# Optimization experiments

Measured on AMD Instinct MI355X. Metric: run time of the kernel, lower is better.

The kernel has to match this reference:

```python
import jax, jax.numpy as jnp
import numpy as np

L, E, NH, V, BS = 8, 1024, 16, 32000, 1024  # layers, embed, heads, vocab, block_size
HD = E // NH  # head dim = 64
FF = 4 * E


def layernorm(x, scale, bias, eps=1e-5):
    mu = jnp.mean(x, axis=-1, keepdims=True)
    var = jnp.var(x, axis=-1, keepdims=True)
    return (x - mu) * jax.lax.rsqrt(var + eps) * scale + bias


def setup_inputs() -> dict:
    key = jax.random.key(0)
    ks = jax.random.split(key, 16)
    s = 0.02
    B, T = 2, 1024
    return {
        "idx": jax.random.randint(ks[0], (B, T), 0, V),
        "tok_emb": jax.random.normal(ks[1], (V, E), jnp.float32) * s,
        "pos_emb": jax.random.normal(ks[2], (BS, E), jnp.float32) * s,
        "Wq": jax.random.normal(ks[3], (L, E, E), jnp.float32) * s,
        "Wk": jax.random.normal(ks[4], (L, E, E), jnp.float32) * s,
        "Wv": jax.random.normal(ks[5], (L, E, E), jnp.float32) * s,
        "Wo": jax.random.normal(ks[6], (L, E, E), jnp.float32) * s,
        "bo": jnp.zeros((L, E), jnp.float32),
        "ln1_s": jnp.ones((L, E), jnp.float32),
        "ln1_b": jnp.zeros((L, E), jnp.float32),
        "W1": jax.random.normal(ks[7], (L, E, FF), jnp.float32) * s,
        "b1": jnp.zeros((L, FF), jnp.float32),
        "W2": jax.random.normal(ks[8], (L, FF, E), jnp.float32) * s,
        "b2": jnp.zeros((L, E), jnp.float32),
        "ln2_s": jnp.ones((L, E), jnp.float32),
        "ln2_b": jnp.zeros((L, E), jnp.float32),
        "lnf_s": jnp.ones((E,), jnp.float32),
        "lnf_b": jnp.zeros((E,), jnp.float32),
        "lm_w": jax.random.normal(ks[9], (E, V), jnp.float32) * s,
        "lm_b": jnp.zeros((V,), jnp.float32),
    }


def reference(idx, tok_emb, pos_emb, Wq, Wk, Wv, Wo, bo, ln1_s, ln1_b,
              W1, b1, W2, b2, ln2_s, ln2_b, lnf_s, lnf_b, lm_w, lm_b):
    B, T = idx.shape
    x = tok_emb[idx] + pos_emb[:T]  # [B,T,E]
    causal = jnp.triu(jnp.ones((T, T), bool), 1)  # True above diagonal -> masked
    scale = 1.0 / jnp.sqrt(jnp.asarray(HD, x.dtype))
    for l in range(L):
        h = layernorm(x, ln1_s[l], ln1_b[l])
        q = (h @ Wq[l]).reshape(B, T, NH, HD)
        k = (h @ Wk[l]).reshape(B, T, NH, HD)
        v = (h @ Wv[l]).reshape(B, T, NH, HD)
        scores = jnp.einsum("bthd,bshd->bhts", q, k) * scale  # [B,H,T,T]
        scores = jnp.where(causal, -jnp.inf, scores)
        attn = jax.nn.softmax(scores, axis=-1)
        o = jnp.einsum("bhts,bshd->bthd", attn, v).reshape(B, T, E)
        x = x + o @ Wo[l] + bo[l]
        h2 = layernorm(x, ln2_s[l], ln2_b[l])
        x = x + jax.nn.gelu(h2 @ W1[l] + b1[l], approximate=False) @ W2[l] + b2[l]
    x = layernorm(x, lnf_s, lnf_b)
    logits = x @ lm_w + lm_b  # [B,T,V]
    return logits
```

## Files before the change

kernel.cpp:

```cpp
#include <hip/hip_runtime.h>

#define EDIM 1024
#define NHEADS 16
#define HDIM 64
#define TSEQ 1024
#define NBATCH 2
#define MROWS 2048
#define FFDIM 4096
#define NLAYERS 8
#define VOCAB 32000
#define QKVN 3072
#define SC2 0.18033688011112042f

typedef __attribute__((ext_vector_type(4))) float f32x4;
typedef __attribute__((ext_vector_type(8))) short short8;

__device__ __forceinline__ unsigned short f2bf(float f) {
    union { float f; unsigned u; } v; v.f = f;
    unsigned r = v.u + 0x7fffu + ((v.u >> 16) & 1u);
    return (unsigned short)(r >> 16);
}

__device__ __forceinline__ f32x4 mfma_bf16(short8 a, short8 b, f32x4 c) {
    return __builtin_amdgcn_mfma_f32_16x16x32_bf16(a, b, c, 0, 0, 0);
}

__device__ __forceinline__ void gload16(const unsigned short* g, unsigned short* l) {
    __builtin_amdgcn_global_load_lds(
        (const __attribute__((address_space(1))) unsigned int*)g,
        (__attribute__((address_space(3))) unsigned int*)l, 16, 0, 0);
}

__device__ __forceinline__ void ln_store(
    f32x4 v, int tid, const float* __restrict__ sc, const float* __restrict__ bi,
    unsigned short* __restrict__ hrow)
{
    float sum = v[0] + v[1] + v[2] + v[3];
    float sq = v[0]*v[0] + v[1]*v[1] + v[2]*v[2] + v[3]*v[3];
    #pragma unroll
    for (int m = 1; m <= 32; m <<= 1) { sum += __shfl_xor(sum, m); sq += __shfl_xor(sq, m); }
    __shared__ float sh[8];
    int w = tid >> 6;
    if ((tid & 63) == 0) { sh[w] = sum; sh[4 + w] = sq; }
    __syncthreads();
    sum = sh[0] + sh[1] + sh[2] + sh[3];
    sq  = sh[4] + sh[5] + sh[6] + sh[7];
    float mu = sum * (1.0f / EDIM);
    float inv = rsqrtf(sq * (1.0f / EDIM) - mu * mu + 1e-5f);
    int c = tid * 4;
    unsigned o0 = (unsigned)f2bf((v[0] - mu) * inv * sc[c + 0] + bi[c + 0])
                | ((unsigned)f2bf((v[1] - mu) * inv * sc[c + 1] + bi[c + 1]) << 16);
    unsigned o1 = (unsigned)f2bf((v[2] - mu) * inv * sc[c + 2] + bi[c + 2])
                | ((unsigned)f2bf((v[3] - mu) * inv * sc[c + 3] + bi[c + 3]) << 16);
    unsigned* hp = (unsigned*)(hrow + c);
    hp[0] = o0; hp[1] = o1;
}

__global__ __launch_bounds__(256) void embed_ln_kernel(
    const int* __restrict__ idx, const float* __restrict__ tok,
    const float* __restrict__ pos, float* __restrict__ x,
    const float* __restrict__ sc, const float* __restrict__ bi,
    unsigned short* __restrict__ h)
{
    int row = blockIdx.x, tid = threadIdx.x;
    int t = row & (TSEQ - 1);
    int tokid = idx[row];
    int c = tid * 4;
    f32x4 a = *(const f32x4*)(tok + (size_t)tokid * EDIM + c);
    f32x4 b = *(const f32x4*)(pos + (size_t)t * EDIM + c);
    f32x4 v = a + b;
    *(f32x4*)(x + (size_t)row * EDIM + c) = v;
    ln_store(v, tid, sc, bi, h + (size_t)row * EDIM);
}

template<int KZ>
__global__ __launch_bounds__(256) void reduce_ln_kernel(
    const float* __restrict__ part, const float* __restrict__ bias,
    float* __restrict__ x, const float* __restrict__ sc,
    const float* __restrict__ bi, unsigned short* __restrict__ h)
{
    int row = blockIdx.x, tid = threadIdx.x;
    int c = tid * 4;
    f32x4 s = *(const f32x4*)(x + (size_t)row * EDIM + c);
    s += *(const f32x4*)(bias + c);
    #pragma unroll
    for (int kz = 0; kz < KZ; ++kz)
        s += *(const f32x4*)(part + ((size_t)kz * MROWS + row) * EDIM + c);
    *(f32x4*)(x + (size_t)row * EDIM + c) = s;
    ln_store(s, tid, sc, bi, h + (size_t)row * EDIM);
}

__device__ __forceinline__ void conv_tile(
    unsigned short* __restrict__ Tb,
    const float* __restrict__ W, unsigned short* __restrict__ WT,
    int Kdim, int Ndim, int k0, int n0, int tid)
{
    int r = tid >> 4, c4 = (tid & 15) * 4;
    #pragma unroll
    for (int i = 0; i < 4; ++i) {
        f32x4 v = *(const f32x4*)(W + (size_t)(k0 + r + 16 * i) * Ndim + n0 + c4);
        Tb[(c4 + 0) * 72 + r + 16 * i] = f2bf(v[0]);
        Tb[(c4 + 1) * 72 + r + 16 * i] = f2bf(v[1]);
        Tb[(c4 + 2) * 72 + r + 16 * i] = f2bf(v[2]);
        Tb[(c4 + 3) * 72 + r + 16 * i] = f2bf(v[3]);
    }
    __syncthreads();
    int nr = tid >> 2, kc = (tid & 3) * 16;
    short8 o0 = *(const short8*)&Tb[nr * 72 + kc];
    short8 o1 = *(const short8*)&Tb[nr * 72 + kc + 8];
    *(short8*)(WT + (size_t)(n0 + nr) * Kdim + k0 + kc)     = o0;
    *(short8*)(WT + (size_t)(n0 + nr) * Kdim + k0 + kc + 8) = o1;
}

__device__ __forceinline__ void wconv_layer_body(
    unsigned short* Tb, int t, int tid,
    const float* Wq, const float* Wk, const float* Wv, const float* Wo,
    const float* W1, const float* W2,
    unsigned short* qkvT, unsigned short* woT,
    unsigned short* w1T, unsigned short* w2T)
{
    if (t < 768) {
        int wsel = t >> 8, tt = t & 255;
        const float* src = wsel == 0 ? Wq : (wsel == 1 ? Wk : Wv);
        conv_tile(Tb, src, qkvT + (size_t)wsel * EDIM * EDIM, EDIM, EDIM,
                  (tt & 15) * 64, (tt >> 4) * 64, tid);
    } else if (t < 1024) {
        int tt = t - 768;
        conv_tile(Tb, Wo, woT, EDIM, EDIM, (tt & 15) * 64, (tt >> 4) * 64, tid);
    } else if (t < 2048) {
        int tt = t - 1024;
        conv_tile(Tb, W1, w1T, EDIM, FFDIM, (tt & 15) * 64, (tt >> 4) * 64, tid);
    } else {
        int tt = t - 2048;
        conv_tile(Tb, W2, w2T, FFDIM, EDIM, (tt >> 4) * 64, (tt & 15) * 64, tid);
    }
}

__global__ __launch_bounds__(256) void wconv_layer_kernel(
    const float* __restrict__ Wq, const float* __restrict__ Wk,
    const float* __restrict__ Wv, const float* __restrict__ Wo,
    const float* __restrict__ W1, const float* __restrict__ W2,
    unsigned short* __restrict__ qkvT, unsigned short* __restrict__ woT,
    unsigned short* __restrict__ w1T, unsigned short* __restrict__ w2T)
{
    __shared__ __align__(16) unsigned short Tb[64 * 72];
    wconv_layer_body(Tb, blockIdx.x, threadIdx.x, Wq, Wk, Wv, Wo, W1, W2,
                     qkvT, woT, w1T, w2T);
}

__global__ __launch_bounds__(256) void wconv_kernel(
    const float* __restrict__ W, unsigned short* __restrict__ WT, int Kdim, int Ndim)
{
    __shared__ __align__(16) unsigned short Tb[64 * 72];
    conv_tile(Tb, W, WT, Kdim, Ndim, blockIdx.x * 64, blockIdx.y * 64, threadIdx.x);
}

template<int EPI>
__device__ __forceinline__ void gemm128_body(
    unsigned short* SMEM,
    const unsigned short* __restrict__ A, const unsigned short* __restrict__ WT,
    float* __restrict__ Cf, unsigned short* __restrict__ Cb,
    int Ndim, int Kdim, int ntiles, int nwg, int kspan, int bid, int kz)
{
    unsigned short* A_lds = SMEM;
    unsigned short* B_lds = SMEM + 8192;
    int tid = threadIdx.x;
    int q8 = nwg >> 3;
    int swz = (bid & 7) * q8 + (bid >> 3);
    int bm0 = (swz / ntiles) * 128, bn0 = (swz % ntiles) * 128;
    int lane = tid & 63, w = tid >> 6;
    int wr = w >> 1, wc = w & 1;
    int r16 = lane & 15, cc = lane >> 4;
    int lrow = lane >> 3;
    int lcol = ((lane & 7) ^ lrow) * 8;
    int sw = r16 & 7;

    f32x4 acc[4][4];
    #pragma unroll
    for (int m = 0; m < 4; ++m)
        #pragma unroll
        for (int n = 0; n < 4; ++n) acc[m][n] = {0.f, 0.f, 0.f, 0.f};

    int kbeg = kz * kspan, kend = kbeg + kspan;
    for (int k0 = kbeg; k0 < kend; k0 += 64) {
        #pragma unroll
        for (int i = 0; i < 4; ++i) {
            int c = i * 4 + w;
            gload16(A + (size_t)(bm0 + c * 8 + lrow) * Kdim + k0 + lcol, A_lds + c * 512);
            gload16(WT + (size_t)(bn0 + c * 8 + lrow) * Kdim + k0 + lcol, B_lds + c * 512);
        }
        __syncthreads();
        #pragma unroll
        for (int kh = 0; kh < 2; ++kh) {
            short8 af[4], bfr[4];
            #pragma unroll
            for (int m = 0; m < 4; ++m)
                af[m] = *(const short8*)&A_lds[(wr * 64 + m * 16 + r16) * 64 + ((kh * 4 + cc) ^ sw) * 8];
            #pragma unroll
            for (int n = 0; n < 4; ++n)
                bfr[n] = *(const short8*)&B_lds[(wc * 64 + n * 16 + r16) * 64 + ((kh * 4 + cc) ^ sw) * 8];
            #pragma unroll
            for (int m = 0; m < 4; ++m)
                #pragma unroll
                for (int n = 0; n < 4; ++n)
                    acc[m][n] = mfma_bf16(af[m], bfr[n], acc[m][n]);
        }
        __syncthreads();
    }

    #pragma unroll
    for (int m = 0; m < 4; ++m) {
        #pragma unroll
        for (int n = 0; n < 4; ++n) {
            #pragma unroll
            for (int j = 0; j < 4; ++j) {
                int row = bm0 + wr * 64 + m * 16 + cc * 4 + j;
                int col = bn0 + wc * 64 + n * 16 + r16;
                float vv = acc[m][n][j];
                if constexpr (EPI == 0)
                    Cb[(size_t)row * Ndim + col] = f2bf(vv);
                else
                    (Cf + (size_t)kz * MROWS * Ndim)[(size_t)row * Ndim + col] = vv;
            }
        }
    }
}

template<int EPI>
__global__ __launch_bounds__(256, 3) void gemm128(
    const unsigned short* __restrict__ A, const unsigned short* __restrict__ WT,
    float* __restrict__ Cf, unsigned short* __restrict__ Cb,
    int Ndim, int Kdim, int ntiles, int nwg, int kspan)
{
    __shared__ __align__(16) unsigned short SMEM[16384];
    gemm128_body<EPI>(SMEM, A, WT, Cf, Cb, Ndim, Kdim, ntiles, nwg, kspan,
                      blockIdx.x, blockIdx.y);
}

template<int MODE>
__global__ __launch_bounds__(256, 3) void ff2_fused_kernel(
    const unsigned short* __restrict__ A, const unsigned short* __restrict__ WT,
    float* __restrict__ Cf,
    const float* __restrict__ Wq, const float* __restrict__ Wk,
    const float* __restrict__ Wv, const float* __restrict__ Wo,
    const float* __restrict__ W1, const float* __restrict__ W2,
    const float* __restrict__ lmW,
    unsigned short* __restrict__ qkvT, unsigned short* __restrict__ woT,
    unsigned short* __restrict__ w1T, unsigned short* __restrict__ w2Tn,
    unsigned short* __restrict__ lmT)
{
    __shared__ __align__(16) unsigned short SMEM[16384];
    int bid = blockIdx.x;
    if (bid < 512) {
        gemm128_body<4>(SMEM, A, WT, Cf, nullptr, EDIM, FFDIM, 8, 128, 1024,
                        bid & 127, bid >> 7);
    } else if constexpr (MODE == 0) {
        wconv_layer_body(SMEM, bid - 512, threadIdx.x, Wq, Wk, Wv, Wo, W1, W2,
                         qkvT, woT, w1T, w2Tn);
    } else {
        int t = bid - 512;
        conv_tile(SMEM, lmW, lmT, EDIM, VOCAB, (t & 15) * 64, (t >> 4) * 64, threadIdx.x);
    }
}

template<int EPI>
__global__ __launch_bounds__(512, 2) void gemm_p3(
    const unsigned short* __restrict__ A, const unsigned short* __restrict__ WT,
    const float* __restrict__ bias, float* __restrict__ Cf,
    unsigned short* __restrict__ Cb, int Ndim, int Kdim, int mtiles, int ntiles)
{
    __shared__ __align__(16) unsigned short LDS[3][24576];
    const int tid = threadIdx.x;
    const int nwg = mtiles * ntiles, q8 = nwg >> 3;
    const int swz = (int)(blockIdx.x & 7) * q8 + (int)(blockIdx.x >> 3);
    const int bn0 = (swz / mtiles) * 256, bm0 = (swz % mtiles) * 128;
    const int lane = tid & 63, w = tid >> 6;
    const int wr = w >> 2, wc = w & 3;
    const int r16 = lane & 15, cc = lane >> 4;
    const int lrow = lane >> 3;
    const int lcol = ((lane & 7) ^ lrow) * 8;
    const int sw = r16 & 7;

    f32x4 acc[4][4];
    #pragma unroll
    for (int m = 0; m < 4; ++m)
        #pragma unroll
        for (int n = 0; n < 4; ++n) acc[m][n] = {0.f, 0.f, 0.f, 0.f};

    const int nk = Kdim >> 6;

    auto STAGE = [&](int t, int bufidx) {
        int k0 = t * 64;
        unsigned short* buf = &LDS[bufidx][0];
        #pragma unroll
        for (int i = 0; i < 2; ++i) {
            int c = i * 8 + w;
            gload16(A + (size_t)(bm0 + c * 8 + lrow) * Kdim + k0 + lcol, buf + c * 512);
        }
        #pragma unroll
        for (int i = 0; i < 4; ++i) {
            int c = i * 8 + w;
            gload16(WT + (size_t)(bn0 + c * 8 + lrow) * Kdim + k0 + lcol, buf + 8192 + c * 512);
        }
    };

    STAGE(0, 0);
    STAGE(1, 1);
    asm volatile("s_waitcnt vmcnt(6)" ::: "memory");
    __builtin_amdgcn_sched_barrier(0);
    __builtin_amdgcn_s_barrier();
    __builtin_amdgcn_sched_barrier(0);

    int cur = 0;
    for (int t = 0; t < nk; ++t) {
        if (t + 2 < nk) STAGE(t + 2, cur == 0 ? 2 : cur - 1);
        const unsigned short* Abuf = &LDS[cur][0];
        const unsigned short* Bbuf = &LDS[cur][8192];
        #pragma unroll
        for (int kh = 0; kh < 2; ++kh) {
            short8 af[4], bfr[4];
            #pragma unroll
            for (int m = 0; m < 4; ++m)
                af[m] = *(const short8*)&Abuf[(wr * 64 + m * 16 + r16) * 64 + ((kh * 4 + cc) ^ sw) * 8];
            #pragma unroll
            for (int n = 0; n < 4; ++n)
                bfr[n] = *(const short8*)&Bbuf[(wc * 64 + n * 16 + r16) * 64 + ((kh * 4 + cc) ^ sw) * 8];
            __builtin_amdgcn_s_setprio(1);
            #pragma unroll
            for (int m = 0; m < 4; ++m)
                #pragma unroll
                for (int n = 0; n < 4; ++n)
                    acc[m][n] = mfma_bf16(af[m], bfr[n], acc[m][n]);
            __builtin_amdgcn_s_setprio(0);
        }
        if (t + 1 < nk) {
            if (t + 2 < nk) asm volatile("s_waitcnt vmcnt(6)" ::: "memory");
            else            asm volatile("s_waitcnt vmcnt(0)" ::: "memory");
            __builtin_amdgcn_sched_barrier(0);
            __builtin_amdgcn_s_barrier();
            __builtin_amdgcn_sched_barrier(0);
            asm volatile("" ::: "memory");
        }
        cur = cur == 2 ? 0 : cur + 1;
    }

    #pragma unroll
    for (int m = 0; m < 4; ++m) {
        #pragma unroll
        for (int n = 0; n < 4; ++n) {
            #pragma unroll
            for (int j = 0; j < 4; ++j) {
                int row = bm0 + wr * 64 + m * 16 + cc * 4 + j;
                int col = bn0 + wc * 64 + n * 16 + r16;
                float vv = acc[m][n][j] + bias[col];
                if constexpr (EPI == 2) {
                    vv = 0.5f * vv * (1.0f + erff(vv * 0.70710678118654752f));
                    Cb[(size_t)row * Ndim + col] = f2bf(vv);
                } else {
                    Cf[(size_t)row * Ndim + col] = vv;
                }
            }
        }
    }
}

__global__ __launch_bounds__(256, 2) void gemm_wide_lm(
    const unsigned short* __restrict__ A, const unsigned short* __restrict__ WT,
    const float* __restrict__ bias, float* __restrict__ Cf,
    int Ndim, int Kdim, int mtiles, int ntiles)
{
    __shared__ __align__(16) unsigned short A_lds[128][64];
    __shared__ __align__(16) unsigned short B_lds[256][64];
    int tid = threadIdx.x;
    int nwg = mtiles * ntiles;
    int q8 = nwg >> 3;
    int swz = (int)(blockIdx.x & 7) * q8 + (int)(blockIdx.x >> 3);
    int bn0 = (swz / mtiles) * 256, bm0 = (swz % mtiles) * 128;
    int lane = tid & 63, w = tid >> 6;
    int wr = w >> 1, wc = w & 1;
    int r16 = lane & 15, cc = lane >> 4;
    int lrow = lane >> 3;
    int lcol = ((lane & 7) ^ lrow) * 8;
    int sw = r16 & 7;

    f32x4 acc[4][8];
    #pragma unroll
    for (int m = 0; m < 4; ++m)
        #pragma unroll
        for (int n = 0; n < 8; ++n) acc[m][n] = {0.f, 0.f, 0.f, 0.f};

    for (int k0 = 0; k0 < Kdim; k0 += 64) {
        #pragma unroll
        for (int i = 0; i < 4; ++i) {
            int c = i * 4 + w;
            gload16(A + (size_t)(bm0 + c * 8 + lrow) * Kdim + k0 + lcol,
                    (unsigned short*)A_lds + c * 512);
        }
        #pragma unroll
        for (int i = 0; i < 8; ++i) {
            int c = i * 4 + w;
            gload16(WT + (size_t)(bn0 + c * 8 + lrow) * Kdim + k0 + lcol,
                    (unsigned short*)B_lds + c * 512);
        }
        __syncthreads();
        #pragma unroll
        for (int kh = 0; kh < 2; ++kh) {
            short8 af[4], bfr[8];
            #pragma unroll
            for (int m = 0; m < 4; ++m)
                af[m] = *(const short8*)&A_lds[wr * 64 + m * 16 + r16][((kh * 4 + cc) ^ sw) * 8];
            #pragma unroll
            for (int n = 0; n < 8; ++n)
                bfr[n] = *(const short8*)&B_lds[wc * 128 + n * 16 + r16][((kh * 4 + cc) ^ sw) * 8];
            #pragma unroll
            for (int m = 0; m < 4; ++m)
                #pragma unroll
                for (int n = 0; n < 8; ++n)
                    acc[m][n] = mfma_bf16(af[m], bfr[n], acc[m][n]);
        }
        __syncthreads();
    }

    #pragma unroll
    for (int m = 0; m < 4; ++m) {
        #pragma unroll
        for (int n = 0; n < 8; ++n) {
            #pragma unroll
            for (int j = 0; j < 4; ++j) {
                int row = bm0 + wr * 64 + m * 16 + cc * 4 + j;
                int col = bn0 + wc * 128 + n * 16 + r16;
                Cf[(size_t)row * Ndim + col] = acc[m][n][j] + bias[col];
            }
        }
    }
}

__global__ __launch_bounds__(256) void attn_kernel(
    const unsigned short* __restrict__ qkv, unsigned short* __restrict__ o)
{
    __shared__ __align__(16) unsigned short K_lds[128][72];
    __shared__ __align__(16) unsigned short VT_lds[64][136];
    __shared__ __align__(16) unsigned short P_lds[4][16][136];

    int qt = (int)gridDim.x - 1 - (int)blockIdx.x;
    int head = blockIdx.y, bb = blockIdx.z;
    int tid = threadIdx.x, w = tid >> 6, lane = tid & 63;
    int r16 = lane & 15, cc = lane >> 4;
    size_t base = ((size_t)bb * TSEQ) * QKVN + head * HDIM;
    const unsigned short* q = qkv + base;
    const unsigned short* k = qkv + base + EDIM;
    const unsigned short* v = qkv + base + 2 * EDIM;
    size_t obase = ((size_t)bb * TSEQ) * EDIM + head * HDIM;
    int qbase = qt * 64;

    const unsigned short* qp = q + (size_t)(qbase + w * 16 + r16) * QKVN;
    short8 aq0 = *(const short8*)(qp + cc * 8);
    short8 aq1 = *(const short8*)(qp + 32 + cc * 8);

    f32x4 oacc[4];
    float m2[4], lrow[4];
    #pragma unroll
    for (int n = 0; n < 4; ++n) oacc[n] = {0.f, 0.f, 0.f, 0.f};
    #pragma unroll
    for (int j = 0; j < 4; ++j) { m2[j] = -1e30f; lrow[j] = 0.f; }

    int krow = tid >> 1, kch = (tid & 1) * 32;
    int vk2 = (tid & 63) * 2, vdb = (tid >> 6) * 16;

    int nkt = (qt + 2) >> 1;
    for (int kt = 0; kt < nkt; ++kt) {
        int kbase = kt * 128;
        const unsigned short* kp = k + (size_t)(kbase + krow) * QKVN + kch;
        *(short8*)&K_lds[krow][kch]      = *(const short8*)kp;
        *(short8*)&K_lds[krow][kch + 8]  = *(const short8*)(kp + 8);
        *(short8*)&K_lds[krow][kch + 16] = *(const short8*)(kp + 16);
        *(short8*)&K_lds[krow][kch + 24] = *(const short8*)(kp + 24);
        const unsigned short* vp0 = v + (size_t)(kbase + vk2) * QKVN + vdb;
        short8 v0a = *(const short8*)vp0;
        short8 v0b = *(const short8*)(vp0 + 8);
        short8 v1a = *(const short8*)(vp0 + QKVN);
        short8 v1b = *(const short8*)(vp0 + QKVN + 8);
        #pragma unroll
        for (int i = 0; i < 8; ++i) {
            *(unsigned*)&VT_lds[vdb + i][vk2] =
                (unsigned)(unsigned short)v0a[i] | ((unsigned)(unsigned short)v1a[i] << 16);
            *(unsigned*)&VT_lds[vdb + 8 + i][vk2] =
                (unsigned)(unsigned short)v0b[i] | ((unsigned)(unsigned short)v1b[i] << 16);
        }
        __syncthreads();

        f32x4 s[8];
        __builtin_amdgcn_s_setprio(1);
        #pragma unroll
        for (int n = 0; n < 8; ++n) {
            short8 bk0 = *(const short8*)&K_lds[n * 16 + r16][cc * 8];
            short8 bk1 = *(const short8*)&K_lds[n * 16 + r16][32 + cc * 8];
            f32x4 z = {0.f, 0.f, 0.f, 0.f};
            z = mfma_bf16(aq0, bk0, z);
            z = mfma_bf16(aq1, bk1, z);
            s[n] = z;
        }
        __builtin_amdgcn_s_setprio(0);
        int myrow = qbase + w * 16 + cc * 4;
        #pragma unroll
        for (int n = 0; n < 8; ++n) {
            int key = kbase + n * 16 + r16;
            #pragma unroll
            for (int j = 0; j < 4; ++j) {
                float sv = s[n][j] * SC2;
                if (key > myrow + j) sv = -1e30f;
                s[n][j] = sv;
            }
        }
        float tmax[4];
        #pragma unroll
        for (int j = 0; j < 4; ++j) {
            float t0 = fmaxf(fmaxf(s[0][j], s[1][j]), fmaxf(s[2][j], s[3][j]));
            float t1 = fmaxf(fmaxf(s[4][j], s[5][j]), fmaxf(s[6][j], s[7][j]));
            float tm = fmaxf(t0, t1);
            #pragma unroll
            for (int mm = 1; mm <= 8; mm <<= 1) tm = fmaxf(tm, __shfl_xor(tm, mm));
            tmax[j] = tm;
        }
        bool defer = (tmax[0] - m2[0] <= 11.5f) && (tmax[1] - m2[1] <= 11.5f)
                  && (tmax[2] - m2[2] <= 11.5f) && (tmax[3] - m2[3] <= 11.5f);
        if (!__all(defer)) {
            #pragma unroll
            for (int j = 0; j < 4; ++j) {
                float mnew = fmaxf(m2[j], tmax[j]);
                float al = exp2f(m2[j] - mnew);
                m2[j] = mnew;
                lrow[j] *= al;
                #pragma unroll
                for (int n = 0; n < 4; ++n) oacc[n][j] *= al;
            }
        }
        #pragma unroll
        for (int j = 0; j < 4; ++j) {
            float ts = 0.f;
            #pragma unroll
            for (int n = 0; n < 8; ++n) {
                float pe = exp2f(s[n][j] - m2[j]);
                s[n][j] = pe;
                ts += pe;
            }
            #pragma unroll
            for (int mm = 1; mm <= 8; mm <<= 1) ts += __shfl_xor(ts, mm);
            lrow[j] += ts;
        }
        #pragma unroll
        for (int n = 0; n < 8; ++n)
            #pragma unroll
            for (int j = 0; j < 4; ++j)
                P_lds[w][cc * 4 + j][n * 16 + r16] = f2bf(s[n][j]);
        short8 pa[4];
        #pragma unroll
        for (int qq = 0; qq < 4; ++qq)
            pa[qq] = *(const short8*)&P_lds[w][r16][qq * 32 + cc * 8];
        __builtin_amdgcn_s_setprio(1);
        #pragma unroll
        for (int n = 0; n < 4; ++n) {
            #pragma unroll
            for (int qq = 0; qq < 4; ++qq) {
                short8 bv = *(const short8*)&VT_lds[n * 16 + r16][qq * 32 + cc * 8];
                oacc[n] = mfma_bf16(pa[qq], bv, oacc[n]);
            }
        }
        __builtin_amdgcn_s_setprio(0);
        __syncthreads();
    }
    float rl[4];
    #pragma unroll
    for (int j = 0; j < 4; ++j) rl[j] = 1.0f / lrow[j];
    #pragma unroll
    for (int n = 0; n < 4; ++n)
        #pragma unroll
        for (int j = 0; j < 4; ++j) {
            int row = qbase + w * 16 + cc * 4 + j;
            o[obase + (size_t)row * EDIM + n * 16 + r16] = f2bf(oacc[n][j] * rl[j]);
        }
}

extern "C" void kernel_launch(void* const* d_in, const int* in_sizes, int n_in,
                              void* d_out, int out_size, void* d_ws, size_t ws_size,
                              hipStream_t stream) {
    const int*   idx     = (const int*)d_in[0];
    const float* tok_emb = (const float*)d_in[1];
    const float* pos_emb = (const float*)d_in[2];
    const float* Wq      = (const float*)d_in[3];
    const float* Wk      = (const float*)d_in[4];
    const float* Wv      = (const float*)d_in[5];
    const float* Wo      = (const float*)d_in[6];
    const float* bo      = (const float*)d_in[7];
    const float* ln1_s   = (const float*)d_in[8];
    const float* ln1_b   = (const float*)d_in[9];
    const float* W1      = (const float*)d_in[10];
    const float* b1      = (const float*)d_in[11];
    const float* W2      = (const float*)d_in[12];
    const float* b2      = (const float*)d_in[13];
    const float* ln2_s   = (const float*)d_in[14];
    const float* ln2_b   = (const float*)d_in[15];
    const float* lnf_s   = (const float*)d_in[16];
    const float* lnf_b   = (const float*)d_in[17];
    const float* lm_w    = (const float*)d_in[18];
    const float* lm_b    = (const float*)d_in[19];
    float* out = (float*)d_out;

    const size_t MB = 1 << 20;
    char* ws = (char*)d_ws;
    float*          x    = (float*)ws;
    unsigned short* h    = (unsigned short*)(ws + 8 * MB);
    unsigned short* qkv  = (unsigned short*)(ws + 12 * MB);
    unsigned short* ao   = (unsigned short*)(ws + 24 * MB);
    unsigned short* ff   = (unsigned short*)(ws + 28 * MB);
    unsigned short* qkvT = (unsigned short*)(ws + 44 * MB);
    unsigned short* woT  = (unsigned short*)(ws + 50 * MB);
    unsigned short* w1T  = (unsigned short*)(ws + 52 * MB);
    unsigned short* w2Ta = (unsigned short*)(ws + 60 * MB);
    unsigned short* lmT  = (unsigned short*)(ws + 68 * MB);

    bool tier1 = ws_size >= (size_t)140 * MB;
    bool tier2 = ws_size >= (size_t)172 * MB;
    unsigned short* w2Tb = tier1 ? (unsigned short*)(ws + 131 * MB) : w2Ta;
    float* part = (float*)(ws + (tier2 ? (size_t)139 * MB : (size_t)68 * MB));

    dim3 blk(256);
    embed_ln_kernel<<<MROWS, blk, 0, stream>>>(idx, tok_emb, pos_emb, x, ln1_s, ln1_b, h);
    wconv_layer_kernel<<<3072, blk, 0, stream>>>(Wq, Wk, Wv, Wo, W1, W2,
                                                 qkvT, woT, w1T, w2Ta);

    for (int l = 0; l < NLAYERS; ++l) {
        unsigned short* w2cur = (l & 1) ? w2Tb : w2Ta;
        unsigned short* w2nxt = ((l + 1) & 1) ? w2Tb : w2Ta;
        size_t eo1 = (size_t)(l + 1) * EDIM * EDIM;

        gemm128<0><<<dim3(384, 1), blk, 0, stream>>>(h, qkvT, nullptr, qkv, QKVN, EDIM, 24, 384, EDIM);
        attn_kernel<<<dim3(TSEQ / 64, NHEADS, NBATCH), blk, 0, stream>>>(qkv, ao);
        gemm128<4><<<dim3(128, 4), blk, 0, stream>>>(ao, woT, part, nullptr, EDIM, EDIM, 8, 128, 256);
        reduce_ln_kernel<4><<<MROWS, blk, 0, stream>>>(part, bo + l * EDIM, x, ln2_s + l * EDIM, ln2_b + l * EDIM, h);
        gemm_p3<2><<<dim3(256, 1), dim3(512), 0, stream>>>(h, w1T, b1 + l * FFDIM, nullptr, ff, FFDIM, EDIM, 16, 16);
        if (l < NLAYERS - 1) {
            if (tier1)
                ff2_fused_kernel<0><<<3584, blk, 0, stream>>>(
                    ff, w2cur, part,
                    Wq + eo1, Wk + eo1, Wv + eo1, Wo + eo1,
                    W1 + (size_t)(l + 1) * EDIM * FFDIM, W2 + (size_t)(l + 1) * FFDIM * EDIM,
                    nullptr, qkvT, woT, w1T, w2nxt, nullptr);
            else {
                gemm128<4><<<dim3(128, 4), blk, 0, stream>>>(ff, w2cur, part, nullptr, EDIM, FFDIM, 8, 128, 1024);
                wconv_layer_kernel<<<3072, blk, 0, stream>>>(
                    Wq + eo1, Wk + eo1, Wv + eo1, Wo + eo1,
                    W1 + (size_t)(l + 1) * EDIM * FFDIM, W2 + (size_t)(l + 1) * FFDIM * EDIM,
                    qkvT, woT, w1T, w2nxt);
            }
        } else {
            if (tier2)
                ff2_fused_kernel<1><<<8512, blk, 0, stream>>>(
                    ff, w2cur, part,
                    nullptr, nullptr, nullptr, nullptr, nullptr, nullptr,
                    lm_w, nullptr, nullptr, nullptr, nullptr, lmT);
            else
                gemm128<4><<<dim3(128, 4), blk, 0, stream>>>(ff, w2cur, part, nullptr, EDIM, FFDIM, 8, 128, 1024);
        }
        if (l < NLAYERS - 1)
            reduce_ln_kernel<4><<<MROWS, blk, 0, stream>>>(part, b2 + l * EDIM, x, ln1_s + (l + 1) * EDIM, ln1_b + (l + 1) * EDIM, h);
        else
            reduce_ln_kernel<4><<<MROWS, blk, 0, stream>>>(part, b2 + l * EDIM, x, lnf_s, lnf_b, h);
    }
    if (!tier2)
        wconv_kernel<<<dim3(16, 500), blk, 0, stream>>>(lm_w, lmT, EDIM, VOCAB);
    gemm_wide_lm<<<dim3(2000, 1), blk, 0, stream>>>(h, lmT, lm_b, out, VOCAB, EDIM, 16, 125);
}
```

Measured before the change: 1.455 ms.

## Rewrite LM-head GEMM as 256x256 tile, 8-wave, triple-buffered pipelined kernel

Replaces the 128x256 LM-head GEMM with a 512-thread kernel that computes 256x256 tiles. It streams K in 32-wide slices through a three-stage LDS ring buffer and issues global loads for step t+2 while MFMAs run on step t. It also raises wave priority around the MFMA bursts and uses explicit vmcnt waits with barriers. The goals are more operand reuse per tile and hiding global-load latency behind compute. In exchange it runs one block per CU with a large register footprint, launches fewer workgroups (1000), and depends on the hand-tuned wait counts being correct.

```diff
diff --git a/kernel.cpp b/kernel.cpp
--- a/kernel.cpp
+++ b/kernel.cpp
@@ -364,71 +364,109 @@
     }
 }
 
-__global__ __launch_bounds__(256, 2) void gemm_wide_lm(
+__global__ __launch_bounds__(512, 1) void gemm_8p(
     const unsigned short* __restrict__ A, const unsigned short* __restrict__ WT,
     const float* __restrict__ bias, float* __restrict__ Cf,
     int Ndim, int Kdim, int mtiles, int ntiles)
 {
-    __shared__ __align__(16) unsigned short A_lds[128][64];
-    __shared__ __align__(16) unsigned short B_lds[256][64];
-    int tid = threadIdx.x;
-    int nwg = mtiles * ntiles;
-    int q8 = nwg >> 3;
-    int swz = (int)(blockIdx.x & 7) * q8 + (int)(blockIdx.x >> 3);
-    int bn0 = (swz / mtiles) * 256, bm0 = (swz % mtiles) * 128;
-    int lane = tid & 63, w = tid >> 6;
-    int wr = w >> 1, wc = w & 1;
-    int r16 = lane & 15, cc = lane >> 4;
-    int lrow = lane >> 3;
-    int lcol = ((lane & 7) ^ lrow) * 8;
-    int sw = r16 & 7;
-
-    f32x4 acc[4][8];
-    #pragma unroll
-    for (int m = 0; m < 4; ++m)
-        #pragma unroll
-        for (int n = 0; n < 8; ++n) acc[m][n] = {0.f, 0.f, 0.f, 0.f};
-
-    for (int k0 = 0; k0 < Kdim; k0 += 64) {
-        #pragma unroll
-        for (int i = 0; i < 4; ++i) {
-            int c = i * 4 + w;
-            gload16(A + (size_t)(bm0 + c * 8 + lrow) * Kdim + k0 + lcol,
-                    (unsigned short*)A_lds + c * 512);
-        }
-        #pragma unroll
-        for (int i = 0; i < 8; ++i) {
-            int c = i * 4 + w;
-            gload16(WT + (size_t)(bn0 + c * 8 + lrow) * Kdim + k0 + lcol,
-                    (unsigned short*)B_lds + c * 512);
-        }
-        __syncthreads();
-        #pragma unroll
-        for (int kh = 0; kh < 2; ++kh) {
-            short8 af[4], bfr[8];
-            #pragma unroll
-            for (int m = 0; m < 4; ++m)
-                af[m] = *(const short8*)&A_lds[wr * 64 + m * 16 + r16][((kh * 4 + cc) ^ sw) * 8];
-            #pragma unroll
-            for (int n = 0; n < 8; ++n)
-                bfr[n] = *(const short8*)&B_lds[wc * 128 + n * 16 + r16][((kh * 4 + cc) ^ sw) * 8];
-            #pragma unroll
-            for (int m = 0; m < 4; ++m)
-                #pragma unroll
-                for (int n = 0; n < 8; ++n)
-                    acc[m][n] = mfma_bf16(af[m], bfr[n], acc[m][n]);
-        }
-        __syncthreads();
-    }
-
-    #pragma unroll
-    for (int m = 0; m < 4; ++m) {
-        #pragma unroll
-        for (int n = 0; n < 8; ++n) {
+    __shared__ __align__(16) unsigned short LDS[3][16384];
+    const int tid = threadIdx.x;
+    const int nwg = mtiles * ntiles, q8 = nwg >> 3;
+    const int swz = (int)(blockIdx.x & 7) * q8 + (int)(blockIdx.x >> 3);
+    const int bn0 = (swz / mtiles) * 256, bm0 = (swz % mtiles) * 256;
+    const int lane = tid & 63, w = tid >> 6;
+    const int wr = w >> 2, wc = w & 3;
+    const int r16 = lane & 15, cc = lane >> 4;
+
+    f32x4 acc[8][4];
+    #pragma unroll
+    for (int m = 0; m < 8; ++m)
+        #pragma unroll
+        for (int n = 0; n < 4; ++n) acc[m][n] = {0.f, 0.f, 0.f, 0.f};
+
+    const int nk = Kdim >> 5;
+
+    #pragma unroll
+    for (int tt = 0; tt < 2; ++tt) {
+        int k0 = tt * 32;
+        unsigned short* buf = &LDS[tt][0];
+        #pragma unroll
+        for (int i = 0; i < 2; ++i) {
+            int c = w * 2 + i;
+            gload16(A  + (size_t)(bm0 + c * 16 + r16) * Kdim + k0 + cc * 8, buf + c * 512);
+            gload16(WT + (size_t)(bn0 + c * 16 + r16) * Kdim + k0 + cc * 8, buf + 8192 + c * 512);
+        }
+    }
+    asm volatile("s_waitcnt vmcnt(4)" ::: "memory");
+    __builtin_amdgcn_sched_barrier(0);
+    __builtin_amdgcn_s_barrier();
+    __builtin_amdgcn_sched_barrier(0);
+
+    int cur = 0;
+    for (int t = 0; t < nk; ++t) {
+        const unsigned short* Abuf = &LDS[cur][0];
+        const unsigned short* Bbuf = &LDS[cur][8192];
+        int nxt = cur + 2; if (nxt >= 3) nxt -= 3;
+        int k2 = (t + 2) * 32;
+        short8 bf[4], af0[4];
+        #pragma unroll
+        for (int n = 0; n < 4; ++n)
+            bf[n] = *(const short8*)(Bbuf + (wc * 4 + n) * 512 + lane * 8);
+        #pragma unroll
+        for (int m = 0; m < 4; ++m)
+            af0[m] = *(const short8*)(Abuf + (wr * 8 + m) * 512 + lane * 8);
+        if (t + 2 < nk) {
+            unsigned short* buf = &LDS[nxt][0];
+            #pragma unroll
+            for (int i = 0; i < 2; ++i) {
+                int c = w * 2 + i;
+                gload16(A + (size_t)(bm0 + c * 16 + r16) * Kdim + k2 + cc * 8, buf + c * 512);
+            }
+        }
+        __builtin_amdgcn_s_setprio(1);
+        #pragma unroll
+        for (int m = 0; m < 4; ++m)
+            #pragma unroll
+            for (int n = 0; n < 4; ++n)
+                acc[m][n] = mfma_bf16(af0[m], bf[n], acc[m][n]);
+        __builtin_amdgcn_s_setprio(0);
+        short8 af1[4];
+        #pragma unroll
+        for (int m = 0; m < 4; ++m)
+            af1[m] = *(const short8*)(Abuf + (wr * 8 + 4 + m) * 512 + lane * 8);
+        if (t + 2 < nk) {
+            unsigned short* buf = &LDS[nxt][8192];
+            #pragma unroll
+            for (int i = 0; i < 2; ++i) {
+                int c = w * 2 + i;
+                gload16(WT + (size_t)(bn0 + c * 16 + r16) * Kdim + k2 + cc * 8, buf + c * 512);
+            }
+        }
+        __builtin_amdgcn_s_setprio(1);
+        #pragma unroll
+        for (int m = 0; m < 4; ++m)
+            #pragma unroll
+            for (int n = 0; n < 4; ++n)
+                acc[4 + m][n] = mfma_bf16(af1[m], bf[n], acc[4 + m][n]);
+        __builtin_amdgcn_s_setprio(0);
+        if (t + 1 < nk) {
+            if (t + 2 < nk) asm volatile("s_waitcnt vmcnt(4)" ::: "memory");
+            else            asm volatile("s_waitcnt vmcnt(0)" ::: "memory");
+            __builtin_amdgcn_sched_barrier(0);
+            __builtin_amdgcn_s_barrier();
+            __builtin_amdgcn_sched_barrier(0);
+        }
+        cur = cur + 1; if (cur >= 3) cur -= 3;
+    }
+
+    #pragma unroll
+    for (int m = 0; m < 8; ++m) {
+        #pragma unroll
+        for (int n = 0; n < 4; ++n) {
             #pragma unroll
             for (int j = 0; j < 4; ++j) {
-                int row = bm0 + wr * 64 + m * 16 + cc * 4 + j;
-                int col = bn0 + wc * 128 + n * 16 + r16;
+                int row = bm0 + wr * 128 + m * 16 + cc * 4 + j;
+                int col = bn0 + wc * 64 + n * 16 + r16;
                 Cf[(size_t)row * Ndim + col] = acc[m][n][j] + bias[col];
             }
         }
@@ -669,5 +707,5 @@
     }
     if (!tier2)
         wconv_kernel<<<dim3(16, 500), blk, 0, stream>>>(lm_w, lmT, EDIM, VOCAB);
-    gemm_wide_lm<<<dim3(2000, 1), blk, 0, stream>>>(h, lmT, lm_b, out, VOCAB, EDIM, 16, 125);
-}
+    gemm_8p<<<dim3(1000, 1), dim3(512), 0, stream>>>(h, lmT, lm_b, out, VOCAB, EDIM, 8, 125);
+}
```

After: 1.460 ms. Within noise of the previous version (+0.3%).
